# Performance work log

Hardware: AMD Instinct MI355X
Metric: run time of the kernel (lower is better)

Reference implementation:

```python
import jax, jax.numpy as jnp
import numpy as np

Q_MAX = 127.0  # int8 dynamic-quant range per npu_dynamic_quant semantics


def setup_inputs() -> dict:
    key = jax.random.key(0)
    kx, kh = jax.random.split(key)
    m, n, k = 8192, 8192, 64
    x = jax.random.normal(kx, (m, n), dtype=jnp.float32)
    h = jax.random.normal(kh, (k, k), dtype=jnp.float32)
    return {"x": x, "h": h}


def reference(x, h):
    m, n = x.shape
    k = h.shape[0]
    # block-diagonal transform: each contiguous k-chunk of every row of x is
    # multiplied by the k x k matrix h
    r = (x.reshape(m * (n // k), k) @ h).reshape(m, n)  # [m, n]
    # dynamic per-row symmetric int8 quantization (npu_dynamic_quant)
    absmax = jnp.max(jnp.abs(r), axis=-1, keepdims=True)  # [m, 1]
    scale = absmax / Q_MAX
    scale = jnp.where(scale == 0, jnp.float32(1.0), scale)  # guard all-zero rows
    y = jnp.clip(jnp.round(r / scale), -128.0, 127.0).astype(jnp.int8)
    return y
```

## Files before the change

kernel.cpp:

```cpp
#include <hip/hip_runtime.h>


typedef _Float16 half8_t __attribute__((ext_vector_type(8)));
typedef float float4_t __attribute__((ext_vector_type(4)));

constexpr int Ncols  = 8192;
constexpr int Kdim   = 64;
constexpr int NWAVES = 4;

__global__ __launch_bounds__(256, 4)
void bdq_mfma(const float* __restrict__ x,
              const float* __restrict__ h,
              int* __restrict__ out)
{
    __shared__ float swmax[NWAVES];

    const int tid  = threadIdx.x;
    const int lane = tid & 63;
    const int wave = tid >> 6;
    const int quad = lane >> 4;
    const int l16  = lane & 15;
    const int row  = blockIdx.x;

    half8_t bfrag[2][4];
#pragma unroll
    for (int ks = 0; ks < 2; ++ks)
#pragma unroll
        for (int ct = 0; ct < 4; ++ct) {
            const int k0  = ks * 32 + quad * 8;
            const int col = ct * 16 + l16;
            half8_t b;
#pragma unroll
            for (int j = 0; j < 8; ++j)
                b[j] = (_Float16)h[(k0 + j) * Kdim + col];
            bfrag[ks][ct] = b;
        }

    const float* xrow = x + (size_t)row * Ncols;

    float4_t acc[2][4];
#pragma unroll
    for (int rt = 0; rt < 2; ++rt)
#pragma unroll
        for (int ct = 0; ct < 4; ++ct)
            acc[rt][ct] = (float4_t){0.f, 0.f, 0.f, 0.f};

#pragma unroll
    for (int rt = 0; rt < 2; ++rt) {
#pragma unroll
        for (int ks = 0; ks < 2; ++ks) {
            const int chunk = wave * 32 + rt * 16 + l16;
            const int k0    = ks * 32 + quad * 8;
            const float4* p = (const float4*)(xrow + chunk * Kdim + k0);
            float4 v0 = p[0], v1 = p[1];
            half8_t a;
            a[0] = (_Float16)v0.x; a[1] = (_Float16)v0.y;
            a[2] = (_Float16)v0.z; a[3] = (_Float16)v0.w;
            a[4] = (_Float16)v1.x; a[5] = (_Float16)v1.y;
            a[6] = (_Float16)v1.z; a[7] = (_Float16)v1.w;
#pragma unroll
            for (int ct = 0; ct < 4; ++ct)
                acc[rt][ct] = __builtin_amdgcn_mfma_f32_16x16x32_f16(
                    a, bfrag[ks][ct], acc[rt][ct], 0, 0, 0);
        }
    }

    float lmax = 0.0f;
#pragma unroll
    for (int rt = 0; rt < 2; ++rt)
#pragma unroll
        for (int ct = 0; ct < 4; ++ct)
#pragma unroll
            for (int i = 0; i < 4; ++i)
                lmax = fmaxf(lmax, fabsf(acc[rt][ct][i]));
#pragma unroll
    for (int off = 32; off > 0; off >>= 1)
        lmax = fmaxf(lmax, __shfl_xor(lmax, off, 64));
    if (lane == 0) swmax[wave] = lmax;
    __syncthreads();

    const float rmax = fmaxf(fmaxf(swmax[0], swmax[1]),
                             fmaxf(swmax[2], swmax[3]));
    const float inv = (rmax > 0.f) ? (127.0f / rmax) : 0.0f;

    int* orow = out + (size_t)row * Ncols;
#pragma unroll
    for (int rt = 0; rt < 2; ++rt)
#pragma unroll
        for (int ct = 0; ct < 4; ++ct)
#pragma unroll
            for (int i = 0; i < 4; ++i) {
                const int chunk = wave * 32 + rt * 16 + quad * 4 + i;
                const int col   = ct * 16 + l16;
                float q = rintf(acc[rt][ct][i] * inv);
                q = fminf(fmaxf(q, -128.f), 127.f);
                orow[chunk * Kdim + col] = (int)q;
            }
}

extern "C" void kernel_launch(void* const* d_in, const int* in_sizes, int n_in,
                              void* d_out, int out_size, void* d_ws, size_t ws_size,
                              hipStream_t stream) {
    const float* x = (const float*)d_in[0];
    const float* h = (const float*)d_in[1];
    int* out = (int*)d_out;
    dim3 grid(8192), block(256);
    hipLaunchKernelGGL(bdq_mfma, grid, block, 0, stream, x, h, out);
}
```

Before: 438.1 us.

## Process four rows per block with prefetch, LDS-staged h, and vectorized stores

Each block now handles four rows. It stages h once into padded LDS as transposed fp16, which amortizes the per-row reload of h from global memory. The next row's x is prefetched into registers while the current row is computed. MFMA operands are swapped so the output layout lets each lane write 16-byte int4 stores instead of scattered 4-byte stores, and the max-reduction scratch is double-buffered to avoid an extra barrier. The cost is more register pressure and fewer blocks in flight.

After: 437.2 us. No clear change (-0.2%).

```diff
diff --git a/kernel.cpp b/kernel.cpp
--- a/kernel.cpp
+++ b/kernel.cpp
@@ -3,99 +3,151 @@
 
 typedef _Float16 half8_t __attribute__((ext_vector_type(8)));
 typedef float float4_t __attribute__((ext_vector_type(4)));
+typedef int int4_t __attribute__((ext_vector_type(4)));
 
 constexpr int Ncols  = 8192;
 constexpr int Kdim   = 64;
 constexpr int NWAVES = 4;
+constexpr int ROWS   = 4;
+constexpr int HPAD   = 72;
+
+#define LDS_BARRIER() do {                                   \
+    asm volatile("s_waitcnt lgkmcnt(0)" ::: "memory");       \
+    __builtin_amdgcn_s_barrier();                            \
+    asm volatile("" ::: "memory");                           \
+} while (0)
 
 __global__ __launch_bounds__(256, 4)
-void bdq_mfma(const float* __restrict__ x,
-              const float* __restrict__ h,
-              int* __restrict__ out)
+void bdq_mfma2(const float* __restrict__ x,
+               const float* __restrict__ h,
+               int* __restrict__ out)
 {
-    __shared__ float swmax[NWAVES];
+    __shared__ __align__(16) _Float16 hT[Kdim * HPAD];
+    __shared__ float swmax[2][NWAVES];
 
-    const int tid  = threadIdx.x;
-    const int lane = tid & 63;
-    const int wave = tid >> 6;
-    const int quad = lane >> 4;
-    const int l16  = lane & 15;
-    const int row  = blockIdx.x;
+    const int tid    = threadIdx.x;
+    const int lane   = tid & 63;
+    const int wave   = tid >> 6;
+    const int quad   = lane >> 4;
+    const int l16    = lane & 15;
+    const int chunk0 = wave * 32;
+    const size_t row0 = (size_t)blockIdx.x * ROWS;
 
-    half8_t bfrag[2][4];
-#pragma unroll
-    for (int ks = 0; ks < 2; ++ks)
-#pragma unroll
-        for (int ct = 0; ct < 4; ++ct) {
-            const int k0  = ks * 32 + quad * 8;
-            const int col = ct * 16 + l16;
-            half8_t b;
-#pragma unroll
-            for (int j = 0; j < 8; ++j)
-                b[j] = (_Float16)h[(k0 + j) * Kdim + col];
-            bfrag[ks][ct] = b;
-        }
+    const float* xr = x + row0 * Ncols;
 
-    const float* xrow = x + (size_t)row * Ncols;
-
-    float4_t acc[2][4];
+    float4 P[2][2][2];
 #pragma unroll
     for (int rt = 0; rt < 2; ++rt)
 #pragma unroll
-        for (int ct = 0; ct < 4; ++ct)
-            acc[rt][ct] = (float4_t){0.f, 0.f, 0.f, 0.f};
+        for (int ks = 0; ks < 2; ++ks) {
+            const float* p = xr + (chunk0 + rt * 16 + l16) * Kdim + ks * 32 + quad * 8;
+            P[rt][ks][0] = ((const float4*)p)[0];
+            P[rt][ks][1] = ((const float4*)p)[1];
+        }
+
+    {
+        const int kk = tid >> 2;
+        const int c0 = (tid & 3) << 4;
+        const float* hp = h + kk * Kdim + c0;
+        float4 v[4];
+#pragma unroll
+        for (int i = 0; i < 4; ++i) v[i] = ((const float4*)hp)[i];
+#pragma unroll
+        for (int i = 0; i < 4; ++i) {
+            hT[(c0 + i * 4 + 0) * HPAD + kk] = (_Float16)v[i].x;
+            hT[(c0 + i * 4 + 1) * HPAD + kk] = (_Float16)v[i].y;
+            hT[(c0 + i * 4 + 2) * HPAD + kk] = (_Float16)v[i].z;
+            hT[(c0 + i * 4 + 3) * HPAD + kk] = (_Float16)v[i].w;
+        }
+    }
+    LDS_BARRIER();
 
 #pragma unroll
-    for (int rt = 0; rt < 2; ++rt) {
+    for (int r = 0; r < ROWS; ++r) {
+        half8_t af[2][2];
 #pragma unroll
-        for (int ks = 0; ks < 2; ++ks) {
-            const int chunk = wave * 32 + rt * 16 + l16;
-            const int k0    = ks * 32 + quad * 8;
-            const float4* p = (const float4*)(xrow + chunk * Kdim + k0);
-            float4 v0 = p[0], v1 = p[1];
-            half8_t a;
-            a[0] = (_Float16)v0.x; a[1] = (_Float16)v0.y;
-            a[2] = (_Float16)v0.z; a[3] = (_Float16)v0.w;
-            a[4] = (_Float16)v1.x; a[5] = (_Float16)v1.y;
-            a[6] = (_Float16)v1.z; a[7] = (_Float16)v1.w;
+        for (int rt = 0; rt < 2; ++rt)
+#pragma unroll
+            for (int ks = 0; ks < 2; ++ks) {
+                half8_t a;
+                a[0] = (_Float16)P[rt][ks][0].x;
+                a[1] = (_Float16)P[rt][ks][0].y;
+                a[2] = (_Float16)P[rt][ks][0].z;
+                a[3] = (_Float16)P[rt][ks][0].w;
+                a[4] = (_Float16)P[rt][ks][1].x;
+                a[5] = (_Float16)P[rt][ks][1].y;
+                a[6] = (_Float16)P[rt][ks][1].z;
+                a[7] = (_Float16)P[rt][ks][1].w;
+                af[rt][ks] = a;
+            }
+
+        if (r + 1 < ROWS) {
+            const float* xn = xr + Ncols;
+#pragma unroll
+            for (int rt = 0; rt < 2; ++rt)
+#pragma unroll
+                for (int ks = 0; ks < 2; ++ks) {
+                    const float* p = xn + (chunk0 + rt * 16 + l16) * Kdim + ks * 32 + quad * 8;
+                    P[rt][ks][0] = ((const float4*)p)[0];
+                    P[rt][ks][1] = ((const float4*)p)[1];
+                }
+        }
+
+        float4_t acc[2][4];
+#pragma unroll
+        for (int rt = 0; rt < 2; ++rt)
 #pragma unroll
             for (int ct = 0; ct < 4; ++ct)
-                acc[rt][ct] = __builtin_amdgcn_mfma_f32_16x16x32_f16(
-                    a, bfrag[ks][ct], acc[rt][ct], 0, 0, 0);
+                acc[rt][ct] = (float4_t){0.f, 0.f, 0.f, 0.f};
+
+#pragma unroll
+        for (int ks = 0; ks < 2; ++ks)
+#pragma unroll
+            for (int ct = 0; ct < 4; ++ct) {
+                const half8_t hf =
+                    *(const half8_t*)&hT[(ct * 16 + l16) * HPAD + ks * 32 + quad * 8];
+#pragma unroll
+                for (int rt = 0; rt < 2; ++rt)
+                    acc[rt][ct] = __builtin_amdgcn_mfma_f32_16x16x32_f16(
+                        hf, af[rt][ks], acc[rt][ct], 0, 0, 0);
+            }
+
+        float lmax = 0.0f;
+#pragma unroll
+        for (int rt = 0; rt < 2; ++rt)
+#pragma unroll
+            for (int ct = 0; ct < 4; ++ct)
+#pragma unroll
+                for (int i = 0; i < 4; ++i)
+                    lmax = fmaxf(lmax, fabsf(acc[rt][ct][i]));
+#pragma unroll
+        for (int off = 32; off > 0; off >>= 1)
+            lmax = fmaxf(lmax, __shfl_xor(lmax, off, 64));
+        if (lane == 0) swmax[r & 1][wave] = lmax;
+        LDS_BARRIER();
+        const float rmax = fmaxf(fmaxf(swmax[r & 1][0], swmax[r & 1][1]),
+                                 fmaxf(swmax[r & 1][2], swmax[r & 1][3]));
+        const float inv = (rmax > 0.f) ? (127.0f / rmax) : 0.0f;
+
+        int* orow = out + (row0 + r) * Ncols;
+#pragma unroll
+        for (int rt = 0; rt < 2; ++rt) {
+            const int cbase = (chunk0 + rt * 16 + l16) * Kdim;
+#pragma unroll
+            for (int ct = 0; ct < 4; ++ct) {
+                int4_t q;
+#pragma unroll
+                for (int i = 0; i < 4; ++i) {
+                    float v = rintf(acc[rt][ct][i] * inv);
+                    v = fminf(fmaxf(v, -128.f), 127.f);
+                    q[i] = (int)v;
+                }
+                *(int4_t*)(orow + cbase + ct * 16 + quad * 4) = q;
+            }
         }
+
+        xr += Ncols;
     }
-
-    float lmax = 0.0f;
-#pragma unroll
-    for (int rt = 0; rt < 2; ++rt)
-#pragma unroll
-        for (int ct = 0; ct < 4; ++ct)
-#pragma unroll
-            for (int i = 0; i < 4; ++i)
-                lmax = fmaxf(lmax, fabsf(acc[rt][ct][i]));
-#pragma unroll
-    for (int off = 32; off > 0; off >>= 1)
-        lmax = fmaxf(lmax, __shfl_xor(lmax, off, 64));
-    if (lane == 0) swmax[wave] = lmax;
-    __syncthreads();
-
-    const float rmax = fmaxf(fmaxf(swmax[0], swmax[1]),
-                             fmaxf(swmax[2], swmax[3]));
-    const float inv = (rmax > 0.f) ? (127.0f / rmax) : 0.0f;
-
-    int* orow = out + (size_t)row * Ncols;
-#pragma unroll
-    for (int rt = 0; rt < 2; ++rt)
-#pragma unroll
-        for (int ct = 0; ct < 4; ++ct)
-#pragma unroll
-            for (int i = 0; i < 4; ++i) {
-                const int chunk = wave * 32 + rt * 16 + quad * 4 + i;
-                const int col   = ct * 16 + l16;
-                float q = rintf(acc[rt][ct][i] * inv);
-                q = fminf(fmaxf(q, -128.f), 127.f);
-                orow[chunk * Kdim + col] = (int)q;
-            }
 }
 
 extern "C" void kernel_launch(void* const* d_in, const int* in_sizes, int n_in,
@@ -104,6 +156,6 @@
     const float* x = (const float*)d_in[0];
     const float* h = (const float*)d_in[1];
     int* out = (int*)d_out;
-    dim3 grid(8192), block(256);
-    hipLaunchKernelGGL(bdq_mfma, grid, block, 0, stream, x, h, out);
+    dim3 grid(8192 / ROWS), block(256);
+    hipLaunchKernelGGL(bdq_mfma2, grid, block, 0, stream, x, h, out);
 }
```
